# Performance work log

Measured on AMD Instinct MI355X. Metric: run time of the kernel, lower is better.

The kernel has to match this reference:

```python
import jax, jax.numpy as jnp
import numpy as np

D_MODEL = 2048
N_HEADS = 32
N_KV_HEADS = 8
HEAD_DIM = D_MODEL // N_HEADS  # 64
N_REP = N_HEADS // N_KV_HEADS  # 4
SCALE = HEAD_DIM ** -0.5


def _rope_tables(seq_len):
    inv_freq = 1.0 / (10000.0 ** (jnp.arange(0, HEAD_DIM, 2, dtype=jnp.float32) / HEAD_DIM))
    t = jnp.arange(seq_len, dtype=jnp.float32)
    freqs = jnp.outer(t, inv_freq)  # [S, HEAD_DIM/2]
    return jnp.cos(freqs), jnp.sin(freqs)


def _apply_rope(x, cos, sin):
    # x: [b, h, s, d]; interleaved even/odd rotation, matching torch stack+flatten
    x_r, x_i = x[..., ::2], x[..., 1::2]
    out_r = x_r * cos - x_i * sin
    out_i = x_r * sin + x_i * cos
    out = jnp.stack([out_r, out_i], axis=-1)  # [b,h,s,d/2,2]
    return out.reshape(x.shape)


def setup_inputs() -> dict:
    key = jax.random.key(0)
    ks = jax.random.split(key, 5)
    bs, seq_len = 2, 2048
    std = D_MODEL ** -0.5
    x = jax.random.normal(ks[0], (bs, seq_len, D_MODEL), dtype=jnp.float32)
    wq = jax.random.normal(ks[1], (N_HEADS * HEAD_DIM, D_MODEL), dtype=jnp.float32) * std
    wk = jax.random.normal(ks[2], (N_KV_HEADS * HEAD_DIM, D_MODEL), dtype=jnp.float32) * std
    wv = jax.random.normal(ks[3], (N_KV_HEADS * HEAD_DIM, D_MODEL), dtype=jnp.float32) * std
    wo = jax.random.normal(ks[4], (D_MODEL, N_HEADS * HEAD_DIM), dtype=jnp.float32) * std
    return {"x": x, "wq": wq, "wk": wk, "wv": wv, "wo": wo}


def reference(x, wq, wk, wv, wo):
    bs, seq_len, _ = x.shape
    # fused-style QKV projections (nn.Linear: x @ W.T)
    q = (x @ wq.T).reshape(bs, seq_len, N_HEADS, HEAD_DIM).transpose(0, 2, 1, 3)
    k = (x @ wk.T).reshape(bs, seq_len, N_KV_HEADS, HEAD_DIM).transpose(0, 2, 1, 3)
    v = (x @ wv.T).reshape(bs, seq_len, N_KV_HEADS, HEAD_DIM).transpose(0, 2, 1, 3)
    cos, sin = _rope_tables(seq_len)  # [S, HEAD_DIM/2], broadcast over b,h
    q = _apply_rope(q, cos, sin)
    k = _apply_rope(k, cos, sin)
    # GQA: repeat KV heads to match Q heads
    k = jnp.repeat(k, N_REP, axis=1)  # [b, H, s, d]
    v = jnp.repeat(v, N_REP, axis=1)
    attn = jnp.einsum('bhqd,bhkd->bhqk', q, k) * SCALE
    causal = jnp.triu(jnp.ones((seq_len, seq_len), dtype=bool), k=1)
    attn = jnp.where(causal, -jnp.inf, attn)
    attn = jax.nn.softmax(attn, axis=-1)
    out = jnp.einsum('bhqk,bhkd->bhqd', attn, v)
    out = out.transpose(0, 2, 1, 3).reshape(bs, seq_len, D_MODEL)
    return out @ wo.T
```

## Files before the change

### kernel.cpp

```cpp
#include <hip/hip_runtime.h>

#define SEQ    2048
#define DM     2048
#define QKVN   3072
#define VTR    64

typedef short s16x8 __attribute__((ext_vector_type(8)));
typedef float f32x4 __attribute__((ext_vector_type(4)));
typedef unsigned short us;

#define MFMA(a,b,c) __builtin_amdgcn_mfma_f32_16x16x32_bf16((a),(b),(c),0,0,0)

__device__ __forceinline__ float bf2f(us u) {
    unsigned v = ((unsigned)u) << 16;
    return __builtin_bit_cast(float, v);
}
__device__ __forceinline__ us f2bf(float f) {
    unsigned u = __builtin_bit_cast(unsigned, f);
    u += 0x7FFFu + ((u >> 16) & 1u);
    return (us)(u >> 16);
}
__device__ __forceinline__ void stp(us* p, float f) {
    *p = (us)(__builtin_bit_cast(unsigned, f) >> 16);
}
__device__ __forceinline__ void glds16(const us* g, us* l) {
    __builtin_amdgcn_global_load_lds((__attribute__((address_space(1))) void*)g,
                                     (__attribute__((address_space(3))) void*)l, 16, 0, 0);
}

__global__ __launch_bounds__(256) void cvt_all(const float* __restrict__ x,
                                               const float* __restrict__ wq,
                                               const float* __restrict__ wk,
                                               const float* __restrict__ wv,
                                               const float* __restrict__ wo,
                                               us* __restrict__ xb,
                                               us* __restrict__ wdst) {
    int i = blockIdx.x * blockDim.x + threadIdx.x;
    const float* src;
    us* dst;
    int off;
    if (i < 2097152)      { src = x;  dst = xb;   off = 0; }
    else {
        int j = i - 2097152;
        dst = wdst;
        if (j < 1048576)      { src = wq; off = 2097152; }
        else if (j < 1310720) { src = wk; off = 2097152 + 1048576; }
        else if (j < 1572864) { src = wv; off = 2097152 + 1310720; }
        else                  { src = wo; off = 2097152 + 1572864; }
    }
    float4 v = ((const float4*)src)[i - off];
    ushort4 o;
    o.x = f2bf(v.x); o.y = f2bf(v.y); o.z = f2bf(v.z); o.w = f2bf(v.w);
    ((ushort4*)(i < 2097152 ? xb : wdst))[i < 2097152 ? i : i - 2097152] = o;
}

template <typename OutT, bool ROPE>
__global__ __launch_bounds__(256) void gemm_bt(const us* __restrict__ A, const us* __restrict__ W,
                                               OutT* __restrict__ C, int M, int N, int K) {
    __shared__ us la[128 * 32];
    __shared__ us lb[128 * 32];
    const int tid = threadIdx.x, lane = tid & 63, wave = tid >> 6;
    const int quad = lane >> 4, lr = lane & 15;
    const int m0 = blockIdx.x * 128, n0 = blockIdx.y * 128;
    const int wm = (wave & 1) * 64, wn = (wave >> 1) * 64;

    f32x4 acc[4][4] = {};

    const int r0 = wave * 32 + (lane >> 2);
    const int c0 = (lane & 3) * 8;
    const us* ga0 = A + (size_t)(m0 + r0) * K + c0;
    const us* ga1 = A + (size_t)(m0 + r0 + 16) * K + c0;
    const us* gb0 = W + (size_t)(n0 + r0) * K + c0;
    const us* gb1 = W + (size_t)(n0 + r0 + 16) * K + c0;
    us* lpa0 = &la[(wave * 32) * 32];
    us* lpa1 = &la[(wave * 32 + 16) * 32];
    us* lpb0 = &lb[(wave * 32) * 32];
    us* lpb1 = &lb[(wave * 32 + 16) * 32];

    for (int k0 = 0; k0 < K; k0 += 32) {
        glds16(ga0 + k0, lpa0);
        glds16(ga1 + k0, lpa1);
        glds16(gb0 + k0, lpb0);
        glds16(gb1 + k0, lpb1);
        __syncthreads();
        s16x8 af[4], bf[4];
#pragma unroll
        for (int i = 0; i < 4; i++) af[i] = *(const s16x8*)&la[(wm + i * 16 + lr) * 32 + quad * 8];
#pragma unroll
        for (int j = 0; j < 4; j++) bf[j] = *(const s16x8*)&lb[(wn + j * 16 + lr) * 32 + quad * 8];
#pragma unroll
        for (int i = 0; i < 4; i++)
#pragma unroll
            for (int j = 0; j < 4; j++)
                acc[i][j] = MFMA(af[i], bf[j], acc[i][j]);
        __syncthreads();
    }

#pragma unroll
    for (int i = 0; i < 4; i++)
#pragma unroll
        for (int j = 0; j < 4; j++)
#pragma unroll
            for (int r = 0; r < 4; r++) {
                int row = m0 + wm + i * 16 + quad * 4 + r;
                int col = n0 + wn + j * 16 + lr;
                float v = acc[i][j][r];
                if (ROPE && n0 < 2560) {
                    int pair = (col >> 1) & 31;
                    float inv = exp2f((float)pair * (-13.2877124f / 32.0f));
                    float ang = (float)(row & (SEQ - 1)) * inv;
                    float c = __cosf(ang), sn = __sinf(ang);
                    float p = __shfl_xor(v, 1);
                    v = v * c + ((col & 1) ? p * sn : -p * sn);
                }
                if constexpr (sizeof(OutT) == 2)
                    C[(size_t)row * N + col] = f2bf(v);
                else
                    C[(size_t)row * N + col] = v;
            }
}

__global__ __launch_bounds__(256) void transpose_v(const us* __restrict__ qkv, us* __restrict__ vt) {
    __shared__ us tile[64][72];
    const int s0 = blockIdx.x * 64;
    const int bk = blockIdx.y;
    const int b = bk >> 3, kvh = bk & 7;
    const int t = threadIdx.x;
    const int r = t >> 3, cg = (t & 7) * 8;
#pragma unroll
    for (int p = 0; p < 2; p++) {
        int rr = r + p * 32;
        *(s16x8*)&tile[rr][cg] =
            *(const s16x8*)(qkv + (size_t)(b * SEQ + s0 + rr) * QKVN + 2560 + kvh * 64 + cg);
    }
    __syncthreads();
#pragma unroll
    for (int p = 0; p < 2; p++) {
        int d = r + p * 32;
        s16x8 val;
#pragma unroll
        for (int u = 0; u < 8; u++) val[u] = tile[cg + u][d];
        *(s16x8*)(vt + ((size_t)bk * VTR + d) * SEQ + s0 + cg) = val;
    }
}

__global__ __launch_bounds__(256, 2) void flash_attn(const us* __restrict__ qkv,
                                                     const us* __restrict__ vt,
                                                     us* __restrict__ o) {
    __shared__ us P[4][4][16 * 72];
    const int bh = blockIdx.y, b = bh >> 5, h = bh & 31, kvh = h >> 2;
    const int wave = threadIdx.x >> 6, lane = threadIdx.x & 63;
    const int quad = lane >> 4, lr = lane & 15;
    const int p = ((int)blockIdx.x + (int)(blockIdx.y >> 3)) & 7;
    const int qts[4] = {p, 15 - p, 16 + p, 31 - p};
    const us* kbase = qkv + (size_t)b * SEQ * QKVN + 2048 + kvh * 64;
    const us* vb = vt + (size_t)(b * 8 + kvh) * VTR * SEQ;
    const float QS = 0.125f * 1.44269504f;

    s16x8 onesb;
    const short ov = (lr == 0) ? (short)0x3F80 : (short)0;
#pragma unroll
    for (int j = 0; j < 8; j++) onesb[j] = ov;

    int q0[4];
    s16x8 qa[4][2];
#pragma unroll
    for (int t = 0; t < 4; t++) {
        q0[t] = qts[t] * 64 + wave * 16;
        const us* qb = qkv + (size_t)(b * SEQ + q0[t]) * QKVN + h * 64;
        qa[t][0] = *(const s16x8*)(qb + (size_t)lr * QKVN + quad * 8);
        qa[t][1] = *(const s16x8*)(qb + (size_t)lr * QKVN + 32 + quad * 8);
#pragma unroll
        for (int j = 0; j < 8; j++) {
            qa[t][0][j] = (short)f2bf(bf2f((us)qa[t][0][j]) * QS);
            qa[t][1][j] = (short)f2bf(bf2f((us)qa[t][1][j]) * QS);
        }
    }

    f32x4 oacc[4][5] = {};
    s16x8 kf[8];
    {
        const us* kp = kbase + (size_t)lr * QKVN;
#pragma unroll
        for (int nb = 0; nb < 4; nb++) {
            kf[2 * nb]     = *(const s16x8*)(kp + (size_t)nb * 16 * QKVN + quad * 8);
            kf[2 * nb + 1] = *(const s16x8*)(kp + (size_t)nb * 16 * QKVN + 32 + quad * 8);
        }
    }

    auto qk_tile = [&](int t, f32x4* sc) {
        __builtin_amdgcn_s_setprio(1);
#pragma unroll
        for (int nb = 0; nb < 4; nb++) {
            sc[nb] = f32x4{0.f, 0.f, 0.f, 0.f};
            sc[nb] = MFMA(qa[t][0], kf[2 * nb], sc[nb]);
            sc[nb] = MFMA(qa[t][1], kf[2 * nb + 1], sc[nb]);
        }
        __builtin_amdgcn_s_setprio(0);
    };
    auto store_tile = [&](int t, const f32x4* sc, int kb) {
        us* Pt = &P[wave][t][0];
        if (kb == qts[t]) {
#pragma unroll
            for (int nb = 0; nb < 4; nb++)
#pragma unroll
                for (int r = 0; r < 4; r++) {
                    int key = kb * 64 + nb * 16 + lr, row = q0[t] + quad * 4 + r;
                    float s = (key > row) ? -1e30f : sc[nb][r];
                    stp(&Pt[(quad * 4 + r) * 72 + nb * 16 + lr], exp2f(s));
                }
        } else {
#pragma unroll
            for (int nb = 0; nb < 4; nb++)
#pragma unroll
                for (int r = 0; r < 4; r++)
                    stp(&Pt[(quad * 4 + r) * 72 + nb * 16 + lr], exp2f(sc[nb][r]));
        }
    };

    const int kbmax = qts[3];
    for (int kb = 0; kb <= kbmax; kb++) {
        const bool a0 = (kb <= qts[0]), a1 = (kb <= qts[1]), a2 = (kb <= qts[2]);
        f32x4 sa[4], sb[4];
        if (a0) qk_tile(0, sa);
        if (a1) qk_tile(1, sb);
        s16x8 vf[8];
#pragma unroll
        for (int n = 0; n < 4; n++)
#pragma unroll
            for (int kc = 0; kc < 2; kc++)
                vf[n * 2 + kc] = *(const s16x8*)(vb + (size_t)(n * 16 + lr) * SEQ +
                                                 kb * 64 + kc * 32 + quad * 8);
        if (a0) store_tile(0, sa, kb);
        if (a1) store_tile(1, sb, kb);
        if (a2) qk_tile(2, sa);
        qk_tile(3, sb);
        if (kb < kbmax) {
            const us* kp = kbase + (size_t)((kb + 1) * 64 + lr) * QKVN;
#pragma unroll
            for (int nb = 0; nb < 4; nb++) {
                kf[2 * nb]     = *(const s16x8*)(kp + (size_t)nb * 16 * QKVN + quad * 8);
                kf[2 * nb + 1] = *(const s16x8*)(kp + (size_t)nb * 16 * QKVN + 32 + quad * 8);
            }
        }
        if (a2) store_tile(2, sa, kb);
        store_tile(3, sb, kb);
        asm volatile("s_waitcnt lgkmcnt(0)" ::: "memory");
        __builtin_amdgcn_s_setprio(1);
#pragma unroll
        for (int t = 0; t < 4; t++) {
            if (kb <= qts[t]) {
#pragma unroll
                for (int kc = 0; kc < 2; kc++) {
                    s16x8 pa = *(const s16x8*)&P[wave][t][lr * 72 + kc * 32 + quad * 8];
#pragma unroll
                    for (int n = 0; n < 4; n++)
                        oacc[t][n] = MFMA(pa, vf[n * 2 + kc], oacc[t][n]);
                    oacc[t][4] = MFMA(pa, onesb, oacc[t][4]);
                }
            }
        }
        __builtin_amdgcn_s_setprio(0);
    }

#pragma unroll
    for (int t = 0; t < 4; t++)
#pragma unroll
        for (int r = 0; r < 4; r++) {
            float l = __shfl(oacc[t][4][r], lane & 48);
            float li = 1.0f / l;
#pragma unroll
            for (int n = 0; n < 4; n++)
                o[(size_t)(b * SEQ + q0[t] + quad * 4 + r) * DM + h * 64 + n * 16 + lr] =
                    f2bf(oacc[t][n][r] * li);
        }
}

extern "C" void kernel_launch(void* const* d_in, const int* in_sizes, int n_in,
                              void* d_out, int out_size, void* d_ws, size_t ws_size,
                              hipStream_t stream) {
    const float* x  = (const float*)d_in[0];
    const float* wq = (const float*)d_in[1];
    const float* wk = (const float*)d_in[2];
    const float* wv = (const float*)d_in[3];
    const float* wo = (const float*)d_in[4];
    float* out = (float*)d_out;

    char* ws = (char*)d_ws;
    const size_t MB = 1024 * 1024;
    us* xb     = (us*)(ws + 0 * MB);
    us* abuf   = (us*)(ws + 0 * MB);
    us* wqkvb  = (us*)(ws + 16 * MB);
    us* wob    = (us*)(ws + 28 * MB);
    us* qkvbuf = (us*)(ws + 36 * MB);
    us* vtbuf  = (us*)(ws + 60 * MB);

    dim3 blk(256);
    cvt_all<<<dim3(18432), blk, 0, stream>>>(x, wq, wk, wv, wo, xb, wqkvb);

    gemm_bt<us, true><<<dim3(32, 24), blk, 0, stream>>>(xb, wqkvb, qkvbuf, 4096, 3072, 2048);
    transpose_v<<<dim3(32, 16), blk, 0, stream>>>(qkvbuf, vtbuf);
    flash_attn<<<dim3(8, 64), blk, 0, stream>>>(qkvbuf, vtbuf, abuf);
    gemm_bt<float, false><<<dim3(32, 16), blk, 0, stream>>>(abuf, wob, out, 4096, 2048, 2048);
}
```

Baseline: 384.9 us.

## Double-buffer K and V fragments across key blocks in attention loop

Restructures the attention key-block loop into a 2x unrolled ping-pong that prefetches both the K and V register fragments for the next block before computing the current one. Previously V was loaded inside the iteration and only K was prefetched, so V load latency sat on the critical path. It also drops the setprio toggling around the QK MFMAs and removes an unused variable in the convert kernel. The extra register buffers raise VGPR pressure and may reduce occupancy or cause spills.

New measurement: 455.4 us. 18.3% more time.

```diff
diff --git a/kernel.cpp b/kernel.cpp
--- a/kernel.cpp
+++ b/kernel.cpp
@@ -37,12 +37,10 @@
                                                us* __restrict__ wdst) {
     int i = blockIdx.x * blockDim.x + threadIdx.x;
     const float* src;
-    us* dst;
     int off;
-    if (i < 2097152)      { src = x;  dst = xb;   off = 0; }
+    if (i < 2097152)      { src = x;  off = 0; }
     else {
         int j = i - 2097152;
-        dst = wdst;
         if (j < 1048576)      { src = wq; off = 2097152; }
         else if (j < 1310720) { src = wk; off = 2097152 + 1048576; }
         else if (j < 1572864) { src = wv; off = 2097152 + 1310720; }
@@ -178,25 +176,29 @@
     }
 
     f32x4 oacc[4][5] = {};
-    s16x8 kf[8];
-    {
-        const us* kp = kbase + (size_t)lr * QKVN;
+
+    auto load_kv = [&](int kb, s16x8* kf, s16x8* vf) {
+        const us* kp = kbase + (size_t)(kb * 64 + lr) * QKVN;
 #pragma unroll
         for (int nb = 0; nb < 4; nb++) {
             kf[2 * nb]     = *(const s16x8*)(kp + (size_t)nb * 16 * QKVN + quad * 8);
             kf[2 * nb + 1] = *(const s16x8*)(kp + (size_t)nb * 16 * QKVN + 32 + quad * 8);
         }
-    }
-
-    auto qk_tile = [&](int t, f32x4* sc) {
-        __builtin_amdgcn_s_setprio(1);
+#pragma unroll
+        for (int n = 0; n < 4; n++)
+#pragma unroll
+            for (int kc = 0; kc < 2; kc++)
+                vf[n * 2 + kc] = *(const s16x8*)(vb + (size_t)(n * 16 + lr) * SEQ +
+                                                 kb * 64 + kc * 32 + quad * 8);
+    };
+
+    auto qk_tile = [&](int t, f32x4* sc, const s16x8* kf) {
 #pragma unroll
         for (int nb = 0; nb < 4; nb++) {
             sc[nb] = f32x4{0.f, 0.f, 0.f, 0.f};
             sc[nb] = MFMA(qa[t][0], kf[2 * nb], sc[nb]);
             sc[nb] = MFMA(qa[t][1], kf[2 * nb + 1], sc[nb]);
         }
-        __builtin_amdgcn_s_setprio(0);
     };
     auto store_tile = [&](int t, const f32x4* sc, int kb) {
         us* Pt = &P[wave][t][0];
@@ -218,31 +220,15 @@
         }
     };
 
-    const int kbmax = qts[3];
-    for (int kb = 0; kb <= kbmax; kb++) {
+    auto full_iter = [&](int kb, const s16x8* kf, const s16x8* vf) {
         const bool a0 = (kb <= qts[0]), a1 = (kb <= qts[1]), a2 = (kb <= qts[2]);
         f32x4 sa[4], sb[4];
-        if (a0) qk_tile(0, sa);
-        if (a1) qk_tile(1, sb);
-        s16x8 vf[8];
-#pragma unroll
-        for (int n = 0; n < 4; n++)
-#pragma unroll
-            for (int kc = 0; kc < 2; kc++)
-                vf[n * 2 + kc] = *(const s16x8*)(vb + (size_t)(n * 16 + lr) * SEQ +
-                                                 kb * 64 + kc * 32 + quad * 8);
+        if (a0) qk_tile(0, sa, kf);
+        if (a1) qk_tile(1, sb, kf);
         if (a0) store_tile(0, sa, kb);
         if (a1) store_tile(1, sb, kb);
-        if (a2) qk_tile(2, sa);
-        qk_tile(3, sb);
-        if (kb < kbmax) {
-            const us* kp = kbase + (size_t)((kb + 1) * 64 + lr) * QKVN;
-#pragma unroll
-            for (int nb = 0; nb < 4; nb++) {
-                kf[2 * nb]     = *(const s16x8*)(kp + (size_t)nb * 16 * QKVN + quad * 8);
-                kf[2 * nb + 1] = *(const s16x8*)(kp + (size_t)nb * 16 * QKVN + 32 + quad * 8);
-            }
-        }
+        if (a2) qk_tile(2, sa, kf);
+        qk_tile(3, sb, kf);
         if (a2) store_tile(2, sa, kb);
         store_tile(3, sb, kb);
         asm volatile("s_waitcnt lgkmcnt(0)" ::: "memory");
@@ -261,6 +247,18 @@
             }
         }
         __builtin_amdgcn_s_setprio(0);
+    };
+
+    s16x8 kfA[8], vfA[8], kfB[8], vfB[8];
+    const int kbmax = qts[3];
+    load_kv(0, kfA, vfA);
+    for (int kb = 0; kb <= kbmax; kb += 2) {
+        if (kb + 1 <= kbmax) load_kv(kb + 1, kfB, vfB);
+        full_iter(kb, kfA, vfA);
+        if (kb + 1 <= kbmax) {
+            if (kb + 2 <= kbmax) load_kv(kb + 2, kfA, vfA);
+            full_iter(kb + 1, kfB, vfB);
+        }
     }
 
 #pragma unroll
```
